# Kernel optimization log

Hardware: AMD Instinct MI355X
Metric: run time of the kernel (lower is better)

Reference implementation:

```python
import jax, jax.numpy as jnp
import numpy as np

D_INP = 4096
D_OUT = 4096
SPARSE_TOP_P = 0.1


def setup_inputs() -> dict:
    key = jax.random.key(0)
    k_x, k_w, k_b = jax.random.split(key, 3)
    x = jax.random.normal(k_x, (4, 2048, D_INP), dtype=jnp.float32)
    full_weight = jax.random.normal(k_w, (D_OUT, D_INP), dtype=jnp.float32) * 0.02
    thresh = jnp.quantile(jnp.abs(full_weight), 1.0 - SPARSE_TOP_P)
    sparse_mask = (jnp.abs(full_weight) >= thresh).astype(jnp.float32)
    sparse_weight = full_weight * sparse_mask
    # bb_kind='matvec': bb_layer.w initialized to the dense remainder, flattened
    bb_w = (full_weight * (1.0 - sparse_mask)).reshape(-1)
    bias = jax.random.normal(k_b, (D_OUT,), dtype=jnp.float32) * 0.02
    return {"x": x, "sparse_weight": sparse_weight, "sparse_mask": sparse_mask,
            "bb_w": bb_w, "bias": bias}


def reference(x, sparse_weight, sparse_mask, bb_w, bias):
    shape = x.shape
    x2 = x.reshape(-1, shape[-1])                      # [N, d_inp]
    w_sparse = sparse_weight * sparse_mask             # masked weight [d_out, d_inp]
    y_sparse = x2 @ w_sparse.T                         # [N, d_out]
    w_bb = bb_w.reshape(D_OUT, D_INP)                  # matvec bb-layer weight
    y_bb = x2 @ w_bb.T                                 # [N, d_out]
    y = y_sparse + y_bb + bias
    return y.reshape(*shape[:-1], D_OUT)
```

## Files before the change

kernel.cpp:

```cpp
#include <hip/hip_runtime.h>
#include <hip/hip_bf16.h>

#define KK 4096
#define NN 4096

using f32x16 = __attribute__((ext_vector_type(16))) float;
using bf16x8 = __attribute__((ext_vector_type(8))) short;

static __device__ __forceinline__ unsigned short f2bf(float f) {
    union { __hip_bfloat16 h; unsigned short u; } cv;
    cv.h = __float2bfloat16(f);
    return cv.u;
}

__global__ __launch_bounds__(256) void prep_x_kernel(const float4* __restrict__ in,
                                                     ushort4* __restrict__ out, int n4) {
    for (int i = blockIdx.x * blockDim.x + threadIdx.x; i < n4; i += gridDim.x * blockDim.x) {
        float4 a = in[i];
        ushort4 o;
        o.x = f2bf(a.x); o.y = f2bf(a.y); o.z = f2bf(a.z); o.w = f2bf(a.w);
        out[i] = o;
    }
}

__global__ __launch_bounds__(256) void prep_w_kernel(const float4* __restrict__ sw,
                                                     const float4* __restrict__ bb,
                                                     ushort4* __restrict__ out, int n4) {
    for (int i = blockIdx.x * blockDim.x + threadIdx.x; i < n4; i += gridDim.x * blockDim.x) {
        float4 a = sw[i], b = bb[i];
        ushort4 o;
        o.x = f2bf(a.x + b.x);
        o.y = f2bf(a.y + b.y);
        o.z = f2bf(a.z + b.z);
        o.w = f2bf(a.w + b.w);
        out[i] = o;
    }
}

__global__ __launch_bounds__(512, 2) void gemm_8p(const short* __restrict__ A,
                                                  const short* __restrict__ B,
                                                  const float* __restrict__ bias,
                                                  float* __restrict__ C, int M) {
    __shared__ __align__(16) short As[2][2][8192];
    __shared__ __align__(16) short Bs[2][2][8192];

    const int tid  = threadIdx.x;
    const int lane = tid & 63;
    const int w    = tid >> 6;
    const int wr   = w >> 2;
    const int wc   = w & 3;
    const int bh   = wc >> 1;
    const int l31  = lane & 31;
    const int l5   = lane >> 5;
    const int l7   = lane & 7;

    const int bid = blockIdx.x;
    const int swz = (bid & 7) * 64 + (bid >> 3);
    const int bm  = (swz >> 4) * 256;
    const int bn  = (swz & 15) * 256;

    const int srow = lane >> 3;
    const int scol = (l7 ^ srow) * 8;
    const short* Abase = A + (size_t)bm * KK + scol;
    const short* Bbase = B + (size_t)bn * KK + scol;

#define STAGE_A(t, h)                                                                      \
    do {                                                                                   \
        _Pragma("unroll") for (int j = 0; j < 2; ++j) {                                    \
            const int rr = (h) * 128 + (w * 2 + j) * 8 + srow;                             \
            __builtin_amdgcn_global_load_lds(                                              \
                (const __attribute__((address_space(1))) void*)(Abase + (size_t)rr * KK + (t) * 64), \
                (__attribute__((address_space(3))) void*)(&As[(t) & 1][h][(w * 2 + j) * 512]), \
                16, 0, 0);                                                                 \
        }                                                                                  \
    } while (0)
#define STAGE_B(t, h)                                                                      \
    do {                                                                                   \
        _Pragma("unroll") for (int j = 0; j < 2; ++j) {                                    \
            const int rr = (h) * 128 + (w * 2 + j) * 8 + srow;                             \
            __builtin_amdgcn_global_load_lds(                                              \
                (const __attribute__((address_space(1))) void*)(Bbase + (size_t)rr * KK + (t) * 64), \
                (__attribute__((address_space(3))) void*)(&Bs[(t) & 1][h][(w * 2 + j) * 512]), \
                16, 0, 0);                                                                 \
        }                                                                                  \
    } while (0)

#define PH_PRE()                                              \
    __builtin_amdgcn_s_barrier();                             \
    asm volatile("s_waitcnt lgkmcnt(0)" ::: "memory");        \
    __builtin_amdgcn_s_setprio(1)
#define PH_POST()                                             \
    __builtin_amdgcn_s_setprio(0);                            \
    __builtin_amdgcn_s_barrier();                             \
    asm volatile("" ::: "memory")

    f32x16 acc[4][2] = {};
    bf16x8 AF1[2][4], AF2[2][4], BF1[4], BF2[4];

    auto rdA = [&](bf16x8 (&dst)[2][4], int buf, int fmBase) {
#pragma unroll
        for (int fm = 0; fm < 2; ++fm)
#pragma unroll
            for (int ks = 0; ks < 4; ++ks) {
                const int row  = (fmBase + fm) * 32 + l31;
                const int slot = (ks * 2 + l5) ^ l7;
                dst[fm][ks] = *(const bf16x8*)&As[buf][wr][row * 64 + slot * 8];
            }
    };
    auto rdB = [&](bf16x8 (&dst)[4], int buf, int rowBase) {
#pragma unroll
        for (int ks = 0; ks < 4; ++ks) {
            const int row  = rowBase + l31;
            const int slot = (ks * 2 + l5) ^ l7;
            dst[ks] = *(const bf16x8*)&Bs[buf][bh][row * 64 + slot * 8];
        }
    };
    auto mmq = [&](f32x16& a0, f32x16& a1, const bf16x8 (&af)[2][4], const bf16x8 (&bf)[4]) {
#pragma unroll
        for (int ks = 0; ks < 4; ++ks) {
            a0 = __builtin_amdgcn_mfma_f32_32x32x16_bf16(af[0][ks], bf[ks], a0, 0, 0, 0);
            a1 = __builtin_amdgcn_mfma_f32_32x32x16_bf16(af[1][ks], bf[ks], a1, 0, 0, 0);
        }
    };

    const int bRow0 = (wc & 1) * 64;

    STAGE_A(0, 0); STAGE_A(0, 1);
    STAGE_B(0, 0); STAGE_B(0, 1);
    STAGE_B(1, 0); STAGE_B(1, 1);
    asm volatile("s_waitcnt vmcnt(4)" ::: "memory");
    __builtin_amdgcn_s_barrier();
    asm volatile("" ::: "memory");

    const int NITER = KK / 128;
    for (int i = 0; i < NITER; ++i) {
        const int t = 2 * i;
        const bool more = (i < NITER - 1);

        rdA(AF1, 0, 0);
        rdB(BF1, 0, bRow0);
        STAGE_A(t + 1, 0);
        PH_PRE();
        mmq(acc[0][0], acc[1][0], AF1, BF1);
        PH_POST();

        rdB(BF2, 0, bRow0 + 32);
        STAGE_A(t + 1, 1);
        PH_PRE();
        mmq(acc[0][1], acc[1][1], AF1, BF2);
        PH_POST();

        rdA(AF2, 0, 2);
        if (more) STAGE_B(t + 2, 0);
        PH_PRE();
        mmq(acc[2][1], acc[3][1], AF2, BF2);
        PH_POST();

        if (more) STAGE_B(t + 2, 1);
        PH_PRE();
        mmq(acc[2][0], acc[3][0], AF2, BF1);
        __builtin_amdgcn_s_setprio(0);
        if (more) { asm volatile("s_waitcnt vmcnt(4)" ::: "memory"); }
        else      { asm volatile("s_waitcnt vmcnt(0)" ::: "memory"); }
        __builtin_amdgcn_s_barrier();
        asm volatile("" ::: "memory");

        rdA(AF1, 1, 0);
        rdB(BF1, 1, bRow0);
        if (more) STAGE_A(t + 2, 0);
        PH_PRE();
        mmq(acc[0][0], acc[1][0], AF1, BF1);
        PH_POST();

        rdB(BF2, 1, bRow0 + 32);
        if (more) STAGE_A(t + 2, 1);
        PH_PRE();
        mmq(acc[0][1], acc[1][1], AF1, BF2);
        PH_POST();

        rdA(AF2, 1, 2);
        if (more) STAGE_B(t + 3, 0);
        PH_PRE();
        mmq(acc[2][1], acc[3][1], AF2, BF2);
        PH_POST();

        if (more) STAGE_B(t + 3, 1);
        PH_PRE();
        mmq(acc[2][0], acc[3][0], AF2, BF1);
        __builtin_amdgcn_s_setprio(0);
        if (more) { asm volatile("s_waitcnt vmcnt(4)" ::: "memory"); }
        else      { asm volatile("s_waitcnt vmcnt(0)" ::: "memory"); }
        __builtin_amdgcn_s_barrier();
        asm volatile("" ::: "memory");
    }

#undef STAGE_A
#undef STAGE_B
#undef PH_PRE
#undef PH_POST

#pragma unroll
    for (int fn = 0; fn < 2; ++fn) {
        const int col = bn + wc * 64 + fn * 32 + l31;
        const float bv = bias[col];
#pragma unroll
        for (int fm = 0; fm < 4; ++fm) {
#pragma unroll
            for (int r = 0; r < 16; ++r) {
                const int row = bm + wr * 128 + fm * 32 + (r & 3) + 8 * (r >> 2) + 4 * l5;
                C[(size_t)row * NN + col] = acc[fm][fn][r] + bv;
            }
        }
    }
}

__global__ __launch_bounds__(256) void fallback_gemm(const float* __restrict__ X,
                                                     const float* __restrict__ SW,
                                                     const float* __restrict__ SM,
                                                     const float* __restrict__ BB,
                                                     const float* __restrict__ bias,
                                                     float* __restrict__ C,
                                                     int M, int N, int K) {
    __shared__ float Xs[32][33];
    __shared__ float Ws[32][33];
    const int tid = threadIdx.x;
    const int tx = tid & 31;
    const int ty = tid >> 5;
    const int bm = blockIdx.x * 32, bn = blockIdx.y * 32;
    float acc[4] = {0.f, 0.f, 0.f, 0.f};
    for (int kt = 0; kt < K; kt += 32) {
#pragma unroll
        for (int r = 0; r < 4; ++r) {
            const int row = ty + r * 8;
            Xs[row][tx] = X[(size_t)(bm + row) * K + kt + tx];
            const size_t wi = (size_t)(bn + row) * K + kt + tx;
            Ws[row][tx] = SW[wi] * SM[wi] + BB[wi];
        }
        __syncthreads();
#pragma unroll 8
        for (int k = 0; k < 32; ++k) {
            const float wv = Ws[tx][k];
#pragma unroll
            for (int r = 0; r < 4; ++r)
                acc[r] += Xs[ty + r * 8][k] * wv;
        }
        __syncthreads();
    }
#pragma unroll
    for (int r = 0; r < 4; ++r)
        C[(size_t)(bm + ty + r * 8) * N + bn + tx] = acc[r] + bias[bn + tx];
}

extern "C" void kernel_launch(void* const* d_in, const int* in_sizes, int n_in,
                              void* d_out, int out_size, void* d_ws, size_t ws_size,
                              hipStream_t stream) {
    const float* x    = (const float*)d_in[0];
    const float* sw   = (const float*)d_in[1];
    const float* sm   = (const float*)d_in[2];
    const float* bb   = (const float*)d_in[3];
    const float* bias = (const float*)d_in[4];
    float* out = (float*)d_out;

    const int K = 4096;
    const int N = 4096;
    const int M = in_sizes[0] / K;

    const size_t xb_bytes = (size_t)M * K * sizeof(short);
    const size_t wb_bytes = (size_t)N * K * sizeof(short);

    if (ws_size < xb_bytes + wb_bytes || (M % 256) != 0 || in_sizes[1] != N * K) {
        dim3 grid(M / 32, N / 32);
        fallback_gemm<<<grid, 256, 0, stream>>>(x, sw, sm, bb, bias, out, M, N, K);
        return;
    }

    short* xb = (short*)d_ws;
    short* wb = (short*)((char*)d_ws + xb_bytes);

    prep_x_kernel<<<2048, 256, 0, stream>>>((const float4*)x, (ushort4*)xb, (M * K) / 4);
    prep_w_kernel<<<2048, 256, 0, stream>>>((const float4*)sw, (const float4*)bb,
                                            (ushort4*)wb, (N * K) / 4);

    const int nwg = (M / 256) * (N / 256);
    gemm_8p<<<nwg, 512, 0, stream>>>(xb, wb, bias, out, M);
}
```

Measured before the change: 340.5 us.

## Switch GEMM to four waves per block with 128x128 per-wave tiles

The bf16 MFMA GEMM now uses 256 threads (4 waves) per 256x256 block instead of 512 (8 waves). Each wave computes a 128x128 sub-tile with 16 accumulators, so each LDS fragment read feeds more MFMAs. The staging schedule also changes: both A and B are prefetched two k-steps ahead, and the loads are grouped per phase with a larger vmcnt wait. In exchange, register pressure rises sharply (256 accumulator floats per lane), occupancy is limited to one block per CU, and there are fewer waves to hide latency.

New measurement: 372.6 us. 1.09x slower.

```diff
diff --git a/kernel.cpp b/kernel.cpp
--- a/kernel.cpp
+++ b/kernel.cpp
@@ -37,7 +37,7 @@
     }
 }
 
-__global__ __launch_bounds__(512, 2) void gemm_8p(const short* __restrict__ A,
+__global__ __launch_bounds__(256, 1) void gemm_4w(const short* __restrict__ A,
                                                   const short* __restrict__ B,
                                                   const float* __restrict__ bias,
                                                   float* __restrict__ C, int M) {
@@ -47,9 +47,8 @@
     const int tid  = threadIdx.x;
     const int lane = tid & 63;
     const int w    = tid >> 6;
-    const int wr   = w >> 2;
-    const int wc   = w & 3;
-    const int bh   = wc >> 1;
+    const int wr   = w >> 1;
+    const int wc   = w & 1;
     const int l31  = lane & 31;
     const int l5   = lane >> 5;
     const int l7   = lane & 7;
@@ -60,30 +59,48 @@
     const int bn  = (swz & 15) * 256;
 
     const int srow = lane >> 3;
-    const int scol = (l7 ^ srow) * 8;
+    const int scol = ((lane & 7) ^ srow) * 8;
     const short* Abase = A + (size_t)bm * KK + scol;
     const short* Bbase = B + (size_t)bn * KK + scol;
 
-#define STAGE_A(t, h)                                                                      \
+#define STAGE_A(T, H)                                                                      \
     do {                                                                                   \
-        _Pragma("unroll") for (int j = 0; j < 2; ++j) {                                    \
-            const int rr = (h) * 128 + (w * 2 + j) * 8 + srow;                             \
+        _Pragma("unroll") for (int j = 0; j < 4; ++j) {                                    \
+            const int rr = (H) * 128 + j * 32 + w * 8 + srow;                              \
             __builtin_amdgcn_global_load_lds(                                              \
-                (const __attribute__((address_space(1))) void*)(Abase + (size_t)rr * KK + (t) * 64), \
-                (__attribute__((address_space(3))) void*)(&As[(t) & 1][h][(w * 2 + j) * 512]), \
+                (const __attribute__((address_space(1))) void*)(Abase + (size_t)rr * KK + (T) * 64), \
+                (__attribute__((address_space(3))) void*)(&As[(T) & 1][H][(j * 256 + w * 64) * 8]), \
                 16, 0, 0);                                                                 \
         }                                                                                  \
     } while (0)
-#define STAGE_B(t, h)                                                                      \
+#define STAGE_B(T, H)                                                                      \
     do {                                                                                   \
-        _Pragma("unroll") for (int j = 0; j < 2; ++j) {                                    \
-            const int rr = (h) * 128 + (w * 2 + j) * 8 + srow;                             \
+        _Pragma("unroll") for (int j = 0; j < 4; ++j) {                                    \
+            const int rr = (H) * 128 + j * 32 + w * 8 + srow;                              \
             __builtin_amdgcn_global_load_lds(                                              \
-                (const __attribute__((address_space(1))) void*)(Bbase + (size_t)rr * KK + (t) * 64), \
-                (__attribute__((address_space(3))) void*)(&Bs[(t) & 1][h][(w * 2 + j) * 512]), \
+                (const __attribute__((address_space(1))) void*)(Bbase + (size_t)rr * KK + (T) * 64), \
+                (__attribute__((address_space(3))) void*)(&Bs[(T) & 1][H][(j * 256 + w * 64) * 8]), \
                 16, 0, 0);                                                                 \
         }                                                                                  \
     } while (0)
+
+#define RDA(DST, BUF, FMB)                                                                 \
+    _Pragma("unroll") for (int f = 0; f < 2; ++f)                                          \
+        _Pragma("unroll") for (int ks = 0; ks < 4; ++ks)                                   \
+            DST[f][ks] = *(const bf16x8*)&As[BUF][wr][(((FMB) + f) * 32 + l31) * 64 + (((ks * 2 + l5) ^ l7) * 8)]
+#define RDB(DST, BUF, FNB)                                                                 \
+    _Pragma("unroll") for (int f = 0; f < 2; ++f)                                          \
+        _Pragma("unroll") for (int ks = 0; ks < 4; ++ks)                                   \
+            DST[f][ks] = *(const bf16x8*)&Bs[BUF][wc][(((FNB) + f) * 32 + l31) * 64 + (((ks * 2 + l5) ^ l7) * 8)]
+
+#define MMQ(AF, BF, FM0, FN0)                                                              \
+    __builtin_amdgcn_s_setprio(1);                                                         \
+    _Pragma("unroll") for (int ks = 0; ks < 4; ++ks)                                       \
+        _Pragma("unroll") for (int fm = 0; fm < 2; ++fm)                                   \
+            _Pragma("unroll") for (int fn = 0; fn < 2; ++fn)                               \
+                acc[(FM0) + fm][(FN0) + fn] = __builtin_amdgcn_mfma_f32_32x32x16_bf16(     \
+                    AF[fm][ks], BF[fn][ks], acc[(FM0) + fm][(FN0) + fn], 0, 0, 0);         \
+    __builtin_amdgcn_s_setprio(0)
 
 #define PH_PRE()                                              \
     __builtin_amdgcn_s_barrier();                             \
@@ -94,41 +111,12 @@
     __builtin_amdgcn_s_barrier();                             \
     asm volatile("" ::: "memory")
 
-    f32x16 acc[4][2] = {};
-    bf16x8 AF1[2][4], AF2[2][4], BF1[4], BF2[4];
-
-    auto rdA = [&](bf16x8 (&dst)[2][4], int buf, int fmBase) {
-#pragma unroll
-        for (int fm = 0; fm < 2; ++fm)
-#pragma unroll
-            for (int ks = 0; ks < 4; ++ks) {
-                const int row  = (fmBase + fm) * 32 + l31;
-                const int slot = (ks * 2 + l5) ^ l7;
-                dst[fm][ks] = *(const bf16x8*)&As[buf][wr][row * 64 + slot * 8];
-            }
-    };
-    auto rdB = [&](bf16x8 (&dst)[4], int buf, int rowBase) {
-#pragma unroll
-        for (int ks = 0; ks < 4; ++ks) {
-            const int row  = rowBase + l31;
-            const int slot = (ks * 2 + l5) ^ l7;
-            dst[ks] = *(const bf16x8*)&Bs[buf][bh][row * 64 + slot * 8];
-        }
-    };
-    auto mmq = [&](f32x16& a0, f32x16& a1, const bf16x8 (&af)[2][4], const bf16x8 (&bf)[4]) {
-#pragma unroll
-        for (int ks = 0; ks < 4; ++ks) {
-            a0 = __builtin_amdgcn_mfma_f32_32x32x16_bf16(af[0][ks], bf[ks], a0, 0, 0, 0);
-            a1 = __builtin_amdgcn_mfma_f32_32x32x16_bf16(af[1][ks], bf[ks], a1, 0, 0, 0);
-        }
-    };
-
-    const int bRow0 = (wc & 1) * 64;
-
-    STAGE_A(0, 0); STAGE_A(0, 1);
-    STAGE_B(0, 0); STAGE_B(0, 1);
-    STAGE_B(1, 0); STAGE_B(1, 1);
-    asm volatile("s_waitcnt vmcnt(4)" ::: "memory");
+    f32x16 acc[4][4] = {};
+    bf16x8 A01[2][4], A23[2][4], B01[2][4], B23[2][4];
+
+    STAGE_A(0, 0); STAGE_A(0, 1); STAGE_B(0, 0); STAGE_B(0, 1);
+    STAGE_B(1, 0); STAGE_B(1, 1); STAGE_A(1, 0); STAGE_A(1, 1);
+    asm volatile("s_waitcnt vmcnt(16)" ::: "memory");
     __builtin_amdgcn_s_barrier();
     asm volatile("" ::: "memory");
 
@@ -137,58 +125,38 @@
         const int t = 2 * i;
         const bool more = (i < NITER - 1);
 
-        rdA(AF1, 0, 0);
-        rdB(BF1, 0, bRow0);
-        STAGE_A(t + 1, 0);
-        PH_PRE();
-        mmq(acc[0][0], acc[1][0], AF1, BF1);
-        PH_POST();
-
-        rdB(BF2, 0, bRow0 + 32);
-        STAGE_A(t + 1, 1);
-        PH_PRE();
-        mmq(acc[0][1], acc[1][1], AF1, BF2);
-        PH_POST();
-
-        rdA(AF2, 0, 2);
-        if (more) STAGE_B(t + 2, 0);
-        PH_PRE();
-        mmq(acc[2][1], acc[3][1], AF2, BF2);
-        PH_POST();
-
-        if (more) STAGE_B(t + 2, 1);
-        PH_PRE();
-        mmq(acc[2][0], acc[3][0], AF2, BF1);
-        __builtin_amdgcn_s_setprio(0);
-        if (more) { asm volatile("s_waitcnt vmcnt(4)" ::: "memory"); }
+        RDA(A01, 0, 0);
+        RDB(B01, 0, 0);
+        PH_PRE(); MMQ(A01, B01, 0, 0); PH_POST();
+
+        RDB(B23, 0, 2);
+        PH_PRE(); MMQ(A01, B23, 0, 2); PH_POST();
+
+        RDA(A23, 0, 2);
+        if (more) { STAGE_B(t + 2, 0); STAGE_B(t + 2, 1); }
+        PH_PRE(); MMQ(A23, B23, 2, 2); PH_POST();
+
+        if (more) { STAGE_A(t + 2, 0); STAGE_A(t + 2, 1); }
+        PH_PRE(); MMQ(A23, B01, 2, 0);
+        if (more) { asm volatile("s_waitcnt vmcnt(16)" ::: "memory"); }
         else      { asm volatile("s_waitcnt vmcnt(0)" ::: "memory"); }
         __builtin_amdgcn_s_barrier();
         asm volatile("" ::: "memory");
 
-        rdA(AF1, 1, 0);
-        rdB(BF1, 1, bRow0);
-        if (more) STAGE_A(t + 2, 0);
-        PH_PRE();
-        mmq(acc[0][0], acc[1][0], AF1, BF1);
-        PH_POST();
-
-        rdB(BF2, 1, bRow0 + 32);
-        if (more) STAGE_A(t + 2, 1);
-        PH_PRE();
-        mmq(acc[0][1], acc[1][1], AF1, BF2);
-        PH_POST();
-
-        rdA(AF2, 1, 2);
-        if (more) STAGE_B(t + 3, 0);
-        PH_PRE();
-        mmq(acc[2][1], acc[3][1], AF2, BF2);
-        PH_POST();
-
-        if (more) STAGE_B(t + 3, 1);
-        PH_PRE();
-        mmq(acc[2][0], acc[3][0], AF2, BF1);
-        __builtin_amdgcn_s_setprio(0);
-        if (more) { asm volatile("s_waitcnt vmcnt(4)" ::: "memory"); }
+        RDA(A01, 1, 0);
+        RDB(B01, 1, 0);
+        PH_PRE(); MMQ(A01, B01, 0, 0); PH_POST();
+
+        RDB(B23, 1, 2);
+        PH_PRE(); MMQ(A01, B23, 0, 2); PH_POST();
+
+        RDA(A23, 1, 2);
+        if (more) { STAGE_B(t + 3, 0); STAGE_B(t + 3, 1); }
+        PH_PRE(); MMQ(A23, B23, 2, 2); PH_POST();
+
+        if (more) { STAGE_A(t + 3, 0); STAGE_A(t + 3, 1); }
+        PH_PRE(); MMQ(A23, B01, 2, 0);
+        if (more) { asm volatile("s_waitcnt vmcnt(16)" ::: "memory"); }
         else      { asm volatile("s_waitcnt vmcnt(0)" ::: "memory"); }
         __builtin_amdgcn_s_barrier();
         asm volatile("" ::: "memory");
@@ -196,12 +164,15 @@
 
 #undef STAGE_A
 #undef STAGE_B
+#undef RDA
+#undef RDB
+#undef MMQ
 #undef PH_PRE
 #undef PH_POST
 
 #pragma unroll
-    for (int fn = 0; fn < 2; ++fn) {
-        const int col = bn + wc * 64 + fn * 32 + l31;
+    for (int fn = 0; fn < 4; ++fn) {
+        const int col = bn + wc * 128 + fn * 32 + l31;
         const float bv = bias[col];
 #pragma unroll
         for (int fm = 0; fm < 4; ++fm) {
@@ -282,5 +253,5 @@
                                             (ushort4*)wb, (N * K) / 4);
 
     const int nwg = (M / 256) * (N / 256);
-    gemm_8p<<<nwg, 512, 0, stream>>>(xb, wb, bias, out, M);
-}
+    gemm_4w<<<nwg, 256, 0, stream>>>(xb, wb, bias, out, M);
+}
```
